# Performance work log

Hardware: AMD Instinct MI355X
Metric: run time of the kernel (lower is better)

The kernel has to match this reference:

```python
import jax, jax.numpy as jnp
import numpy as np

B, C, H, W = 8, 16, 512, 512


def setup_inputs() -> dict:
    key = jax.random.key(0)
    k1, k2, k3 = jax.random.split(key, 3)
    v = jax.random.normal(k1, (B, C, H, W), dtype=jnp.float32)
    # query coords in pixel units, slightly outside [0, W) / [0, H) to hit the invalid mask
    xq = jax.random.uniform(k2, (B, H, W), dtype=jnp.float32) * (W + 2.0) - 1.0
    yq = jax.random.uniform(k3, (B, H, W), dtype=jnp.float32) * (H + 2.0) - 1.0
    return {"v": v, "xq": xq, "yq": yq}


def reference(v, xq, yq):
    b, c, h, w = v.shape
    x0 = jnp.clip(jnp.floor(xq).astype(jnp.int32), 0, w - 1)
    y0 = jnp.clip(jnp.floor(yq).astype(jnp.int32), 0, h - 1)
    x1 = jnp.clip(x0 + 1, 0, w - 1)
    y1 = jnp.clip(y0 + 1, 0, h - 1)

    # flatten v to (B*H*W, C) like _bchw2bhwc(...).view(-1, C)
    v_flat = jnp.transpose(v, (0, 2, 3, 1)).reshape(-1, c)
    offs = (jnp.arange(b, dtype=jnp.int32) * (h * w))[:, None, None]  # [B,1,1]

    def gather(ys, xs):
        idx = (ys * w + xs + offs).reshape(-1)
        return jnp.take(v_flat, idx, axis=0).reshape(b, h, w, c)

    v00 = gather(y0, x0)
    v01 = gather(y0, x1)
    v10 = gather(y1, x0)
    v11 = gather(y1, x1)

    dx = xq - x0.astype(xq.dtype)  # [B,H,W]
    dy = yq - y0.astype(yq.dtype)
    w00 = ((1.0 - dy) * (1.0 - dx))[..., None]
    w01 = ((1.0 - dy) * dx)[..., None]
    w10 = (dy * (1.0 - dx))[..., None]
    w11 = (dy * dx)[..., None]

    out_bhwc = v00 * w00 + v01 * w01 + v10 * w10 + v11 * w11  # [B,H,W,C]
    values = jnp.transpose(out_bhwc, (0, 3, 1, 2))  # [B,C,H,W]

    invalid = ((xq < 0) | (xq >= w) | (yq < 0) | (yq >= h))[:, None, :, :]
    inv = invalid.astype(values.dtype)
    return inv * jnp.zeros_like(values) + (1.0 - inv) * values
```

## Files before the change

### kernel.cpp

```cpp
#include <hip/hip_runtime.h>
#include <hip/hip_fp16.h>


#define BATCH 8
#define CHAN  16
#define HEIGHT 512
#define WIDTH  512
#define HW (HEIGHT * WIDTH)

__global__ __launch_bounds__(256) void transpose_bchw2bhwc_f16(
    const float* __restrict__ v, __half* __restrict__ vt)
{
    const int tid = blockIdx.x * blockDim.x + threadIdx.x;
    if (tid >= BATCH * HW) return;
    const int b = tid / HW;
    const int p = tid - b * HW;

    const float* src = v + (size_t)b * CHAN * HW + p;

    __half2 d[8];
#pragma unroll
    for (int j = 0; j < 8; ++j) {
        const float lo = __builtin_nontemporal_load(&src[(size_t)(2 * j + 0) * HW]);
        const float hi = __builtin_nontemporal_load(&src[(size_t)(2 * j + 1) * HW]);
        d[j] = __floats2half2_rn(lo, hi);
    }

    uint4* dst = (uint4*)(vt + (size_t)tid * CHAN);
    dst[0] = *(const uint4*)&d[0];
    dst[1] = *(const uint4*)&d[4];
}

__global__ __launch_bounds__(256) void interp2_bhwc_f16(
    const __half* __restrict__ vt,
    const float* __restrict__ xq,
    const float* __restrict__ yq,
    float* __restrict__ out)
{
    const int tid = blockIdx.x * blockDim.x + threadIdx.x;
    if (tid >= BATCH * HW) return;

    const int b   = tid / HW;
    const int pix = tid - b * HW;

    const float xqv = __builtin_nontemporal_load(&xq[tid]);
    const float yqv = __builtin_nontemporal_load(&yq[tid]);

    const bool invalid = (xqv < 0.0f) | (xqv >= (float)WIDTH) |
                         (yqv < 0.0f) | (yqv >= (float)HEIGHT);

    int x0 = (int)floorf(xqv);
    int y0 = (int)floorf(yqv);
    x0 = min(max(x0, 0), WIDTH - 1);
    y0 = min(max(y0, 0), HEIGHT - 1);
    const int x1 = min(x0 + 1, WIDTH - 1);
    const int y1 = min(y0 + 1, HEIGHT - 1);

    const float dx = xqv - (float)x0;
    const float dy = yqv - (float)y0;

    float w00 = (1.0f - dy) * (1.0f - dx);
    float w01 = (1.0f - dy) * dx;
    float w10 = dy * (1.0f - dx);
    float w11 = dy * dx;
    if (invalid) { w00 = 0.0f; w01 = 0.0f; w10 = 0.0f; w11 = 0.0f; }

    const size_t bbase = (size_t)b * HW;

    float acc[CHAN];
#pragma unroll
    for (int c = 0; c < CHAN; ++c) acc[c] = 0.0f;

    auto corner = [&](int y, int x, float w) {
        const __half* p = vt + (bbase + (size_t)y * WIDTH + x) * CHAN;
        const uint4 a0 = *(const uint4*)p;
        const uint4 a1 = *(const uint4*)(p + 8);
        const __half2* h0 = (const __half2*)&a0;
        const __half2* h1 = (const __half2*)&a1;
#pragma unroll
        for (int j = 0; j < 4; ++j) {
            const float2 f = __half22float2(h0[j]);
            acc[2 * j + 0] += w * f.x;
            acc[2 * j + 1] += w * f.y;
        }
#pragma unroll
        for (int j = 0; j < 4; ++j) {
            const float2 f = __half22float2(h1[j]);
            acc[8 + 2 * j + 0] += w * f.x;
            acc[8 + 2 * j + 1] += w * f.y;
        }
    };

    corner(y0, x0, w00);
    corner(y0, x1, w01);
    corner(y1, x0, w10);
    corner(y1, x1, w11);

    const size_t obase = (size_t)b * CHAN * HW + pix;
#pragma unroll
    for (int c = 0; c < CHAN; ++c)
        __builtin_nontemporal_store(acc[c], &out[obase + (size_t)c * HW]);
}

__global__ __launch_bounds__(256) void interp2_bchw(
    const float* __restrict__ v,
    const float* __restrict__ xq,
    const float* __restrict__ yq,
    float* __restrict__ out)
{
    const int tid = blockIdx.x * blockDim.x + threadIdx.x;
    if (tid >= BATCH * HW) return;

    const int b   = tid / HW;
    const int pix = tid - b * HW;

    const float xqv = xq[tid];
    const float yqv = yq[tid];
    const bool invalid = (xqv < 0.0f) | (xqv >= (float)WIDTH) |
                         (yqv < 0.0f) | (yqv >= (float)HEIGHT);

    int x0 = (int)floorf(xqv);
    int y0 = (int)floorf(yqv);
    x0 = min(max(x0, 0), WIDTH - 1);
    y0 = min(max(y0, 0), HEIGHT - 1);
    const int x1 = min(x0 + 1, WIDTH - 1);
    const int y1 = min(y0 + 1, HEIGHT - 1);

    const float dx = xqv - (float)x0;
    const float dy = yqv - (float)y0;
    float w00 = (1.0f - dy) * (1.0f - dx);
    float w01 = (1.0f - dy) * dx;
    float w10 = dy * (1.0f - dx);
    float w11 = dy * dx;
    if (invalid) { w00 = 0.0f; w01 = 0.0f; w10 = 0.0f; w11 = 0.0f; }

    const int off00 = y0 * WIDTH + x0;
    const int off01 = y0 * WIDTH + x1;
    const int off10 = y1 * WIDTH + x0;
    const int off11 = y1 * WIDTH + x1;

    const int vbase = b * CHAN * HW;
    const int obase = vbase + pix;
#pragma unroll
    for (int c = 0; c < CHAN; ++c) {
        const int cb = vbase + c * HW;
        out[obase + c * HW] = v[cb + off00] * w00 + v[cb + off01] * w01 +
                              v[cb + off10] * w10 + v[cb + off11] * w11;
    }
}

extern "C" void kernel_launch(void* const* d_in, const int* in_sizes, int n_in,
                              void* d_out, int out_size, void* d_ws, size_t ws_size,
                              hipStream_t stream) {
    const float* v  = (const float*)d_in[0];
    const float* xq = (const float*)d_in[1];
    const float* yq = (const float*)d_in[2];
    float* out = (float*)d_out;

    const int npix = BATCH * HW;
    const int block = 256;
    const int grid = (npix + block - 1) / block;

    const size_t vt_bytes = (size_t)BATCH * CHAN * HW * sizeof(__half);
    if (ws_size >= vt_bytes) {
        __half* vt = (__half*)d_ws;
        transpose_bchw2bhwc_f16<<<grid, block, 0, stream>>>(v, vt);
        interp2_bhwc_f16<<<grid, block, 0, stream>>>(vt, xq, yq, out);
    } else {
        interp2_bchw<<<grid, block, 0, stream>>>(v, xq, yq, out);
    }
}
```

Before: 129.0 us.

## Split fp16 BHWC staging into two 8-channel planes and interpolate per half

The transpose now writes channels 0-7 and 8-15 into two separate fp16 planes. Interpolation runs as two launches, each gathering one 16-byte chunk per corner. Block indices are interleaved across batches so concurrent blocks cover all batch images. The goal is a smaller gather working set per pass for better L2/MALL hit rates, at the cost of reading xq/yq twice and one extra launch.

```diff
diff --git a/kernel.cpp b/kernel.cpp
--- a/kernel.cpp
+++ b/kernel.cpp
@@ -7,44 +7,46 @@
 #define HEIGHT 512
 #define WIDTH  512
 #define HW (HEIGHT * WIDTH)
+#define BLOCKS_PER_BATCH (HW / 256)
 
-__global__ __launch_bounds__(256) void transpose_bchw2bhwc_f16(
-    const float* __restrict__ v, __half* __restrict__ vt)
+__global__ __launch_bounds__(256) void transpose_split_f16(
+    const float* __restrict__ v, __half* __restrict__ vt0, __half* __restrict__ vt1)
 {
-    const int tid = blockIdx.x * blockDim.x + threadIdx.x;
-    if (tid >= BATCH * HW) return;
-    const int b = tid / HW;
-    const int p = tid - b * HW;
+    const int blk = blockIdx.x;
+    const int b = blk & 7;
+    const int j = blk >> 3;
+    const int p = j * 256 + threadIdx.x;
+    const int tid = b * HW + p;
 
     const float* src = v + (size_t)b * CHAN * HW + p;
 
     __half2 d[8];
 #pragma unroll
-    for (int j = 0; j < 8; ++j) {
-        const float lo = __builtin_nontemporal_load(&src[(size_t)(2 * j + 0) * HW]);
-        const float hi = __builtin_nontemporal_load(&src[(size_t)(2 * j + 1) * HW]);
-        d[j] = __floats2half2_rn(lo, hi);
+    for (int j2 = 0; j2 < 8; ++j2) {
+        const float lo = __builtin_nontemporal_load(&src[(size_t)(2 * j2 + 0) * HW]);
+        const float hi = __builtin_nontemporal_load(&src[(size_t)(2 * j2 + 1) * HW]);
+        d[j2] = __floats2half2_rn(lo, hi);
     }
 
-    uint4* dst = (uint4*)(vt + (size_t)tid * CHAN);
-    dst[0] = *(const uint4*)&d[0];
-    dst[1] = *(const uint4*)&d[4];
+    *(uint4*)(vt0 + (size_t)tid * 8) = *(const uint4*)&d[0];
+    *(uint4*)(vt1 + (size_t)tid * 8) = *(const uint4*)&d[4];
 }
 
-__global__ __launch_bounds__(256) void interp2_bhwc_f16(
-    const __half* __restrict__ vt,
+__global__ __launch_bounds__(256) void interp2_half8(
+    const __half* __restrict__ vth,
     const float* __restrict__ xq,
     const float* __restrict__ yq,
-    float* __restrict__ out)
+    float* __restrict__ out,
+    int c0)
 {
-    const int tid = blockIdx.x * blockDim.x + threadIdx.x;
-    if (tid >= BATCH * HW) return;
+    const int blk = blockIdx.x;
+    const int b = blk & 7;
+    const int j = blk >> 3;
+    const int p = j * 256 + threadIdx.x;
+    const int qidx = b * HW + p;
 
-    const int b   = tid / HW;
-    const int pix = tid - b * HW;
-
-    const float xqv = __builtin_nontemporal_load(&xq[tid]);
-    const float yqv = __builtin_nontemporal_load(&yq[tid]);
+    const float xqv = __builtin_nontemporal_load(&xq[qidx]);
+    const float yqv = __builtin_nontemporal_load(&yq[qidx]);
 
     const bool invalid = (xqv < 0.0f) | (xqv >= (float)WIDTH) |
                          (yqv < 0.0f) | (yqv >= (float)HEIGHT);
@@ -67,27 +69,18 @@
 
     const size_t bbase = (size_t)b * HW;
 
-    float acc[CHAN];
+    float acc[8];
 #pragma unroll
-    for (int c = 0; c < CHAN; ++c) acc[c] = 0.0f;
+    for (int c = 0; c < 8; ++c) acc[c] = 0.0f;
 
     auto corner = [&](int y, int x, float w) {
-        const __half* p = vt + (bbase + (size_t)y * WIDTH + x) * CHAN;
-        const uint4 a0 = *(const uint4*)p;
-        const uint4 a1 = *(const uint4*)(p + 8);
-        const __half2* h0 = (const __half2*)&a0;
-        const __half2* h1 = (const __half2*)&a1;
+        const uint4 a = *(const uint4*)(vth + (bbase + (size_t)y * WIDTH + x) * 8);
+        const __half2* h = (const __half2*)&a;
 #pragma unroll
-        for (int j = 0; j < 4; ++j) {
-            const float2 f = __half22float2(h0[j]);
-            acc[2 * j + 0] += w * f.x;
-            acc[2 * j + 1] += w * f.y;
-        }
-#pragma unroll
-        for (int j = 0; j < 4; ++j) {
-            const float2 f = __half22float2(h1[j]);
-            acc[8 + 2 * j + 0] += w * f.x;
-            acc[8 + 2 * j + 1] += w * f.y;
+        for (int k = 0; k < 4; ++k) {
+            const float2 f = __half22float2(h[k]);
+            acc[2 * k + 0] += w * f.x;
+            acc[2 * k + 1] += w * f.y;
         }
     };
 
@@ -96,9 +89,9 @@
     corner(y1, x0, w10);
     corner(y1, x1, w11);
 
-    const size_t obase = (size_t)b * CHAN * HW + pix;
+    const size_t obase = (size_t)b * CHAN * HW + (size_t)c0 * HW + p;
 #pragma unroll
-    for (int c = 0; c < CHAN; ++c)
+    for (int c = 0; c < 8; ++c)
         __builtin_nontemporal_store(acc[c], &out[obase + (size_t)c * HW]);
 }
 
@@ -157,16 +150,17 @@
     const float* yq = (const float*)d_in[2];
     float* out = (float*)d_out;
 
-    const int npix = BATCH * HW;
-    const int block = 256;
-    const int grid = (npix + block - 1) / block;
+    const int grid = BATCH * BLOCKS_PER_BATCH;
+    const size_t half_bytes = (size_t)BATCH * HW * 8 * sizeof(__half);
 
-    const size_t vt_bytes = (size_t)BATCH * CHAN * HW * sizeof(__half);
-    if (ws_size >= vt_bytes) {
-        __half* vt = (__half*)d_ws;
-        transpose_bchw2bhwc_f16<<<grid, block, 0, stream>>>(v, vt);
-        interp2_bhwc_f16<<<grid, block, 0, stream>>>(vt, xq, yq, out);
+    if (ws_size >= 2 * half_bytes) {
+        __half* vt0 = (__half*)d_ws;
+        __half* vt1 = (__half*)((char*)d_ws + half_bytes);
+        transpose_split_f16<<<grid, 256, 0, stream>>>(v, vt0, vt1);
+        interp2_half8<<<grid, 256, 0, stream>>>(vt0, xq, yq, out, 0);
+        interp2_half8<<<grid, 256, 0, stream>>>(vt1, xq, yq, out, 8);
     } else {
-        interp2_bchw<<<grid, block, 0, stream>>>(v, xq, yq, out);
+        const int npix = BATCH * HW;
+        interp2_bchw<<<(npix + 255) / 256, 256, 0, stream>>>(v, xq, yq, out);
     }
 }
```

New measurement: 134.7 us. 1.04x slower.
